# Performance work log

Measured on AMD Instinct MI355X. Metric: run time of the kernel, lower is better.

The kernel has to match this reference:

```python
import jax, jax.numpy as jnp
import numpy as np

IN_CAP_NUM = 1024
IN_CAP_DIM = 64
OUT_CAP_NUM = 32
OUT_CAP_DIM = 64
BATCH = 64
NUM_ITER = 3


def squash(t):
    # t: [..., d]; scale = |t|^2 / (1+|t|^2) / |t|
    sq = jnp.sum(t * t, axis=-1, keepdims=True)
    scale = sq / (1.0 + sq) / jnp.sqrt(sq)
    return scale * t


def setup_inputs() -> dict:
    key = jax.random.key(0)
    k1, k2 = jax.random.split(key)
    x = jax.random.normal(k1, (IN_CAP_NUM, BATCH, IN_CAP_DIM), dtype=jnp.float32)
    route_w = 0.1 * jax.random.normal(
        k2, (OUT_CAP_NUM, IN_CAP_NUM, IN_CAP_DIM, OUT_CAP_DIM), dtype=jnp.float32)
    return {"x": x, "route_w": route_w}


def reference(x, route_w):
    # u[o,i,b,e] = sum_d x[i,b,d] * route_w[o,i,d,e]  (torch broadcast matmul)
    u = jnp.einsum('ibd,oide->oibe', x, route_w)  # [O, I, B, E]
    O = route_w.shape[0]
    b = jnp.zeros((O, 1, 1, 1), dtype=u.dtype)
    v = None
    for it in range(NUM_ITER):
        c = jax.nn.softmax(b, axis=0)                 # coupling over out caps
        s = jnp.sum(c * u, axis=1)                    # [O, B, E]
        v = squash(s)                                 # [O, B, E]
        if it < NUM_ITER - 1:
            # agreement: [O, I, B, 1]
            b = b + jnp.sum(u * v[:, None, :, :], axis=-1, keepdims=True)
    return v
```

## Files before the change

kernel.cpp:

```cpp
#include <hip/hip_runtime.h>
#include <stdint.h>


#define IC 1024
#define OC 32
#define DD 64
#define EE 64
#define BB 64

typedef __attribute__((ext_vector_type(8))) short short8;
typedef __attribute__((ext_vector_type(16))) float f32x16;
typedef _Float16 half8 __attribute__((ext_vector_type(8)));

__device__ __forceinline__ unsigned short f2bf(float f) {
    unsigned int u = __float_as_uint(f);
    u = (u + 0x7FFFu + ((u >> 16) & 1u)) >> 16;
    return (unsigned short)u;
}
__device__ __forceinline__ unsigned int pk2(float a, float b) {
    return (unsigned int)f2bf(a) | ((unsigned int)f2bf(b) << 16);
}

__global__ __launch_bounds__(256)
void u_gemm_kernel(const float* __restrict__ x,
                   const float* __restrict__ w,
                   _Float16* __restrict__ u,
                   float* __restrict__ s_out)
{
    __shared__ unsigned short xs[64 * 68];
    __shared__ unsigned short wT[64 * 68];
    const int t = threadIdx.x;
    const int o = blockIdx.y;
    const int chunk = blockIdx.x;
    const int lane = t & 63;
    const int wv = t >> 6;
    const int bh = wv & 1, eh = wv >> 1;
    const int seg = t & 7;
    const int rrow = t >> 3;

    f32x16 stot = (f32x16)0.0f;

    for (int ii = 0; ii < 32; ++ii) {
        const int i = chunk * 32 + ii;
        __syncthreads();
        for (int hlf = 0; hlf < 2; ++hlf) {
            const int b = rrow + hlf * 32;
            const float* xp = x + (((size_t)i) * BB + b) * DD + seg * 8;
            const float4 xa = *(const float4*)xp;
            const float4 xb = *(const float4*)(xp + 4);
            uint2* dst = (uint2*)&xs[b * 68 + seg * 8];
            dst[0] = make_uint2(pk2(xa.x, xa.y), pk2(xa.z, xa.w));
            dst[1] = make_uint2(pk2(xb.x, xb.y), pk2(xb.z, xb.w));
        }
        {
            const int d0 = rrow * 2;
            const float* wp = w + ((((size_t)o) * IC + i) * DD + d0) * EE + seg * 8;
            const float4 a0 = *(const float4*)(wp);
            const float4 a1 = *(const float4*)(wp + 4);
            const float4 b0 = *(const float4*)(wp + EE);
            const float4 b1 = *(const float4*)(wp + EE + 4);
            const float r0[8] = {a0.x, a0.y, a0.z, a0.w, a1.x, a1.y, a1.z, a1.w};
            const float r1[8] = {b0.x, b0.y, b0.z, b0.w, b1.x, b1.y, b1.z, b1.w};
            #pragma unroll
            for (int j = 0; j < 8; ++j) {
                const int e = seg * 8 + j;
                *(unsigned int*)&wT[e * 68 + d0] = pk2(r0[j], r1[j]);
            }
        }
        __syncthreads();
        f32x16 acc = (f32x16)0.0f;
        #pragma unroll
        for (int kk = 0; kk < 4; ++kk) {
            const int k0 = kk * 16 + (lane >> 5) * 8;
            const int ar = bh * 32 + (lane & 31);
            const int br = eh * 32 + (lane & 31);
            uint2 alo = *(const uint2*)&xs[ar * 68 + k0];
            uint2 ahi = *(const uint2*)&xs[ar * 68 + k0 + 4];
            uint2 blo = *(const uint2*)&wT[br * 68 + k0];
            uint2 bhi = *(const uint2*)&wT[br * 68 + k0 + 4];
            union { uint4 q; short8 s; } au, bu;
            au.q = make_uint4(alo.x, alo.y, ahi.x, ahi.y);
            bu.q = make_uint4(blo.x, blo.y, bhi.x, bhi.y);
            acc = __builtin_amdgcn_mfma_f32_32x32x16_bf16(au.s, bu.s, acc, 0, 0, 0);
        }
        _Float16* ub = u + ((((size_t)o) * IC + i) * BB) * EE;
        #pragma unroll
        for (int r = 0; r < 16; ++r) {
            const int gb = bh * 32 + (r & 3) + 8 * (r >> 2) + 4 * (lane >> 5);
            const int ge = eh * 32 + (lane & 31);
            ub[gb * EE + ge] = (_Float16)acc[r];
            stot[r] += acc[r];
        }
    }
    #pragma unroll
    for (int r = 0; r < 16; ++r) {
        const int gb = bh * 32 + (r & 3) + 8 * (r >> 2) + 4 * (lane >> 5);
        const int ge = eh * 32 + (lane & 31);
        atomicAdd(&s_out[(((size_t)o) * BB + gb) * EE + ge], stot[r] * (1.0f / 32.0f));
    }
}

template<bool FIRST>
__global__ __launch_bounds__(256)
void logits_kernel(const _Float16* __restrict__ u,
                   const float* __restrict__ v,
                   const float* __restrict__ bprev,
                   float* __restrict__ bout,
                   float* __restrict__ cbuf)
{
    __shared__ float Lp[OC][BB];
    const int t = threadIdx.x;
    const int i = blockIdx.x;
    const int b = t >> 2;
    const int eq = t & 3;

    for (int o = 0; o < OC; ++o) {
        const _Float16* up = u + ((((size_t)o) * IC + i) * BB + b) * EE + eq * 16;
        const float*    vp = v + (((size_t)o) * BB + b) * EE + eq * 16;
        const half8 u0 = *(const half8*)up;
        const half8 u1 = *(const half8*)(up + 8);
        const float4 va = *(const float4*)vp;
        const float4 vb = *(const float4*)(vp + 4);
        const float4 vc = *(const float4*)(vp + 8);
        const float4 vd = *(const float4*)(vp + 12);
        float p = (float)u0[0]*va.x + (float)u0[1]*va.y + (float)u0[2]*va.z + (float)u0[3]*va.w
                + (float)u0[4]*vb.x + (float)u0[5]*vb.y + (float)u0[6]*vb.z + (float)u0[7]*vb.w
                + (float)u1[0]*vc.x + (float)u1[1]*vc.y + (float)u1[2]*vc.z + (float)u1[3]*vc.w
                + (float)u1[4]*vd.x + (float)u1[5]*vd.y + (float)u1[6]*vd.z + (float)u1[7]*vd.w;
        p += __shfl_xor(p, 1);
        p += __shfl_xor(p, 2);
        if (eq == 0) Lp[o][b] = p;
    }
    __syncthreads();
    if (t < BB) {
        const int bb = t;
        float lt[OC];
        float m = -1e30f;
        #pragma unroll
        for (int o = 0; o < OC; ++o) {
            float L = Lp[o][bb];
            if (!FIRST) L += bprev[(((size_t)o) * IC + i) * BB + bb];
            if (FIRST)  bout[(((size_t)o) * IC + i) * BB + bb] = L;
            lt[o] = L;
            m = fmaxf(m, L);
        }
        float Z = 0.f;
        #pragma unroll
        for (int o = 0; o < OC; ++o) { lt[o] = __expf(lt[o] - m); Z += lt[o]; }
        const float rZ = 1.0f / Z;
        #pragma unroll
        for (int o = 0; o < OC; ++o)
            cbuf[(((size_t)o) * IC + i) * BB + bb] = lt[o] * rZ;
    }
}

__global__ __launch_bounds__(256)
void sweight_kernel(const _Float16* __restrict__ u,
                    const float* __restrict__ cbuf,
                    float* __restrict__ s_out)
{
    const int t = threadIdx.x;
    const int chunk = blockIdx.x;
    const int o = blockIdx.y;
    const int b = t >> 2;
    const int eq = t & 3;
    float acc[16];
    #pragma unroll
    for (int j = 0; j < 16; ++j) acc[j] = 0.f;
    const int i0 = chunk * 32;
    for (int ii = 0; ii < 32; ++ii) {
        const int i = i0 + ii;
        const float c = cbuf[(((size_t)o) * IC + i) * BB + b];
        const _Float16* up = u + ((((size_t)o) * IC + i) * BB + b) * EE + eq * 16;
        const half8 u0 = *(const half8*)up;
        const half8 u1 = *(const half8*)(up + 8);
        #pragma unroll
        for (int j = 0; j < 8; ++j) acc[j]     += c * (float)u0[j];
        #pragma unroll
        for (int j = 0; j < 8; ++j) acc[8 + j] += c * (float)u1[j];
    }
    float* sp = s_out + (((size_t)o) * BB + b) * EE + eq * 16;
    #pragma unroll
    for (int j = 0; j < 16; ++j) atomicAdd(&sp[j], acc[j]);
}

__global__ __launch_bounds__(256)
void squash_kernel(const float* __restrict__ s, float* __restrict__ vout)
{
    const int o = blockIdx.x;
    const int lane = threadIdx.x & 63;
    const int wv = threadIdx.x >> 6;
    for (int b = wv; b < BB; b += 4) {
        const size_t idx = (((size_t)o) * BB + b) * EE + lane;
        const float val = s[idx];
        float sq = val * val;
        #pragma unroll
        for (int off = 1; off < 64; off <<= 1)
            sq += __shfl_xor(sq, off);
        const float r = sqrtf(sq);
        vout[idx] = val * (r / (1.0f + sq));
    }
}

extern "C" void kernel_launch(void* const* d_in, const int* in_sizes, int n_in,
                              void* d_out, int out_size, void* d_ws, size_t ws_size,
                              hipStream_t stream)
{
    const float* x = (const float*)d_in[0];
    const float* w = (const float*)d_in[1];
    float* out = (float*)d_out;

    char* ws = (char*)d_ws;
    float*    s_buf = (float*)ws;
    float*    vbuf  = (float*)(ws + (1 << 19));
    float*    b1    = (float*)(ws + (1 << 20));
    float*    cbuf  = (float*)(ws + (1 << 20) + (8 << 20));
    _Float16* u     = (_Float16*)(ws + (17u << 20));

    const dim3 blk(256);

    hipMemsetAsync(s_buf, 0, 1 << 19, stream);
    u_gemm_kernel<<<dim3(32, 32), blk, 0, stream>>>(x, w, u, s_buf);
    squash_kernel<<<32, blk, 0, stream>>>(s_buf, vbuf);
    logits_kernel<true><<<1024, blk, 0, stream>>>(u, vbuf, nullptr, b1, cbuf);
    hipMemsetAsync(s_buf, 0, 1 << 19, stream);
    sweight_kernel<<<dim3(32, 32), blk, 0, stream>>>(u, cbuf, s_buf);
    squash_kernel<<<32, blk, 0, stream>>>(s_buf, vbuf);
    logits_kernel<false><<<1024, blk, 0, stream>>>(u, vbuf, b1, nullptr, cbuf);
    hipMemsetAsync(s_buf, 0, 1 << 19, stream);
    sweight_kernel<<<dim3(32, 32), blk, 0, stream>>>(u, cbuf, s_buf);
    squash_kernel<<<32, blk, 0, stream>>>(s_buf, out);
}
```

Before: 1.415 ms.

## Double-buffer GEMM staging, fuse squash into logits, split sweight chunks

The u GEMM kernel now double-buffers its shared-memory tiles and prefetches the next input's x/w registers while the current tile's MFMAs run. The intermediate squash kernels are removed: the logits kernel recomputes the squash scale from s inline and software-pipelines its per-output loads. The weighted-sum kernel uses 16-input chunks with preloaded coefficients and a doubled grid, giving more parallelism at the cost of more atomics. The trade-offs are higher register pressure and redundant norm computation per block.

```diff
diff --git a/kernel.cpp b/kernel.cpp
--- a/kernel.cpp
+++ b/kernel.cpp
@@ -27,8 +27,8 @@
                    _Float16* __restrict__ u,
                    float* __restrict__ s_out)
 {
-    __shared__ unsigned short xs[64 * 68];
-    __shared__ unsigned short wT[64 * 68];
+    __shared__ unsigned short xs[2][64 * 68];
+    __shared__ unsigned short wT[2][64 * 68];
     const int t = threadIdx.x;
     const int o = blockIdx.y;
     const int chunk = blockIdx.x;
@@ -37,60 +37,73 @@
     const int bh = wv & 1, eh = wv >> 1;
     const int seg = t & 7;
     const int rrow = t >> 3;
+    const int d0 = rrow * 2;
+    const int ar = bh * 32 + (lane & 31);
+    const int br = eh * 32 + (lane & 31);
 
     f32x16 stot = (f32x16)0.0f;
 
-    for (int ii = 0; ii < 32; ++ii) {
-        const int i = chunk * 32 + ii;
+#define LOADSET(i_, X0,X1,X2,X3, W0,W1,W2,W3) do {                          \
+    const float* xp = x + (((size_t)(i_)) * BB + rrow) * DD + seg * 8;      \
+    X0 = *(const float4*)xp;            X1 = *(const float4*)(xp + 4);      \
+    X2 = *(const float4*)(xp + 32*DD);  X3 = *(const float4*)(xp + 32*DD+4);\
+    const float* wp = w + ((((size_t)o) * IC + (i_)) * DD + d0) * EE + seg*8;\
+    W0 = *(const float4*)wp;            W1 = *(const float4*)(wp + 4);      \
+    W2 = *(const float4*)(wp + EE);     W3 = *(const float4*)(wp + EE + 4); \
+} while(0)
+
+#define STAGESET(bf_, X0,X1,X2,X3, W0,W1,W2,W3) do {                        \
+    uint2* dx0 = (uint2*)&xs[bf_][rrow * 68 + seg * 8];                     \
+    dx0[0] = make_uint2(pk2(X0.x, X0.y), pk2(X0.z, X0.w));                  \
+    dx0[1] = make_uint2(pk2(X1.x, X1.y), pk2(X1.z, X1.w));                  \
+    uint2* dx1 = (uint2*)&xs[bf_][(rrow + 32) * 68 + seg * 8];              \
+    dx1[0] = make_uint2(pk2(X2.x, X2.y), pk2(X2.z, X2.w));                  \
+    dx1[1] = make_uint2(pk2(X3.x, X3.y), pk2(X3.z, X3.w));                  \
+    const float r0_[8] = {W0.x,W0.y,W0.z,W0.w,W1.x,W1.y,W1.z,W1.w};         \
+    const float r1_[8] = {W2.x,W2.y,W2.z,W2.w,W3.x,W3.y,W3.z,W3.w};         \
+    _Pragma("unroll")                                                       \
+    for (int j = 0; j < 8; ++j)                                             \
+        *(unsigned int*)&wT[bf_][(seg * 8 + j) * 68 + d0] = pk2(r0_[j], r1_[j]); \
+} while(0)
+
+#define MFMA_STORE(bf_, i_) do {                                            \
+    f32x16 acc = (f32x16)0.0f;                                              \
+    _Pragma("unroll")                                                       \
+    for (int kk = 0; kk < 4; ++kk) {                                        \
+        const int k0 = kk * 16 + (lane >> 5) * 8;                           \
+        uint2 alo = *(const uint2*)&xs[bf_][ar * 68 + k0];                  \
+        uint2 ahi = *(const uint2*)&xs[bf_][ar * 68 + k0 + 4];              \
+        uint2 blo = *(const uint2*)&wT[bf_][br * 68 + k0];                  \
+        uint2 bhi = *(const uint2*)&wT[bf_][br * 68 + k0 + 4];              \
+        union { uint4 q; short8 s; } au, bu;                                \
+        au.q = make_uint4(alo.x, alo.y, ahi.x, ahi.y);                      \
+        bu.q = make_uint4(blo.x, blo.y, bhi.x, bhi.y);                      \
+        acc = __builtin_amdgcn_mfma_f32_32x32x16_bf16(au.s, bu.s, acc, 0, 0, 0); \
+    }                                                                       \
+    _Float16* ubp = u + ((((size_t)o) * IC + (i_)) * BB) * EE;              \
+    _Pragma("unroll")                                                       \
+    for (int r = 0; r < 16; ++r) {                                          \
+        const int gb = bh * 32 + (r & 3) + 8 * (r >> 2) + 4 * (lane >> 5);  \
+        const int ge = eh * 32 + (lane & 31);                               \
+        ubp[gb * EE + ge] = (_Float16)acc[r];                               \
+        stot[r] += acc[r];                                                  \
+    }                                                                       \
+} while(0)
+
+    float4 XA0,XA1,XA2,XA3, WA0,WA1,WA2,WA3;
+    float4 XB0,XB1,XB2,XB3, WB0,WB1,WB2,WB3;
+    const int i0 = chunk * 32;
+    LOADSET(i0, XA0,XA1,XA2,XA3, WA0,WA1,WA2,WA3);
+    for (int ii = 0; ii < 32; ii += 2) {
+        STAGESET(0, XA0,XA1,XA2,XA3, WA0,WA1,WA2,WA3);
+        LOADSET(i0 + ii + 1, XB0,XB1,XB2,XB3, WB0,WB1,WB2,WB3);
         __syncthreads();
-        for (int hlf = 0; hlf < 2; ++hlf) {
-            const int b = rrow + hlf * 32;
-            const float* xp = x + (((size_t)i) * BB + b) * DD + seg * 8;
-            const float4 xa = *(const float4*)xp;
-            const float4 xb = *(const float4*)(xp + 4);
-            uint2* dst = (uint2*)&xs[b * 68 + seg * 8];
-            dst[0] = make_uint2(pk2(xa.x, xa.y), pk2(xa.z, xa.w));
-            dst[1] = make_uint2(pk2(xb.x, xb.y), pk2(xb.z, xb.w));
-        }
-        {
-            const int d0 = rrow * 2;
-            const float* wp = w + ((((size_t)o) * IC + i) * DD + d0) * EE + seg * 8;
-            const float4 a0 = *(const float4*)(wp);
-            const float4 a1 = *(const float4*)(wp + 4);
-            const float4 b0 = *(const float4*)(wp + EE);
-            const float4 b1 = *(const float4*)(wp + EE + 4);
-            const float r0[8] = {a0.x, a0.y, a0.z, a0.w, a1.x, a1.y, a1.z, a1.w};
-            const float r1[8] = {b0.x, b0.y, b0.z, b0.w, b1.x, b1.y, b1.z, b1.w};
-            #pragma unroll
-            for (int j = 0; j < 8; ++j) {
-                const int e = seg * 8 + j;
-                *(unsigned int*)&wT[e * 68 + d0] = pk2(r0[j], r1[j]);
-            }
-        }
+        MFMA_STORE(0, i0 + ii);
+        STAGESET(1, XB0,XB1,XB2,XB3, WB0,WB1,WB2,WB3);
+        if (ii + 2 < 32)
+            LOADSET(i0 + ii + 2, XA0,XA1,XA2,XA3, WA0,WA1,WA2,WA3);
         __syncthreads();
-        f32x16 acc = (f32x16)0.0f;
-        #pragma unroll
-        for (int kk = 0; kk < 4; ++kk) {
-            const int k0 = kk * 16 + (lane >> 5) * 8;
-            const int ar = bh * 32 + (lane & 31);
-            const int br = eh * 32 + (lane & 31);
-            uint2 alo = *(const uint2*)&xs[ar * 68 + k0];
-            uint2 ahi = *(const uint2*)&xs[ar * 68 + k0 + 4];
-            uint2 blo = *(const uint2*)&wT[br * 68 + k0];
-            uint2 bhi = *(const uint2*)&wT[br * 68 + k0 + 4];
-            union { uint4 q; short8 s; } au, bu;
-            au.q = make_uint4(alo.x, alo.y, ahi.x, ahi.y);
-            bu.q = make_uint4(blo.x, blo.y, bhi.x, bhi.y);
-            acc = __builtin_amdgcn_mfma_f32_32x32x16_bf16(au.s, bu.s, acc, 0, 0, 0);
-        }
-        _Float16* ub = u + ((((size_t)o) * IC + i) * BB) * EE;
-        #pragma unroll
-        for (int r = 0; r < 16; ++r) {
-            const int gb = bh * 32 + (r & 3) + 8 * (r >> 2) + 4 * (lane >> 5);
-            const int ge = eh * 32 + (lane & 31);
-            ub[gb * EE + ge] = (_Float16)acc[r];
-            stot[r] += acc[r];
-        }
+        MFMA_STORE(1, i0 + ii + 1);
     }
     #pragma unroll
     for (int r = 0; r < 16; ++r) {
@@ -98,12 +111,15 @@
         const int ge = eh * 32 + (lane & 31);
         atomicAdd(&s_out[(((size_t)o) * BB + gb) * EE + ge], stot[r] * (1.0f / 32.0f));
     }
+#undef LOADSET
+#undef STAGESET
+#undef MFMA_STORE
 }
 
 template<bool FIRST>
 __global__ __launch_bounds__(256)
 void logits_kernel(const _Float16* __restrict__ u,
-                   const float* __restrict__ v,
+                   const float* __restrict__ s,
                    const float* __restrict__ bprev,
                    float* __restrict__ bout,
                    float* __restrict__ cbuf)
@@ -113,23 +129,52 @@
     const int i = blockIdx.x;
     const int b = t >> 2;
     const int eq = t & 3;
-
-    for (int o = 0; o < OC; ++o) {
-        const _Float16* up = u + ((((size_t)o) * IC + i) * BB + b) * EE + eq * 16;
-        const float*    vp = v + (((size_t)o) * BB + b) * EE + eq * 16;
-        const half8 u0 = *(const half8*)up;
-        const half8 u1 = *(const half8*)(up + 8);
-        const float4 va = *(const float4*)vp;
-        const float4 vb = *(const float4*)(vp + 4);
-        const float4 vc = *(const float4*)(vp + 8);
-        const float4 vd = *(const float4*)(vp + 12);
-        float p = (float)u0[0]*va.x + (float)u0[1]*va.y + (float)u0[2]*va.z + (float)u0[3]*va.w
-                + (float)u0[4]*vb.x + (float)u0[5]*vb.y + (float)u0[6]*vb.z + (float)u0[7]*vb.w
-                + (float)u1[0]*vc.x + (float)u1[1]*vc.y + (float)u1[2]*vc.z + (float)u1[3]*vc.w
-                + (float)u1[4]*vd.x + (float)u1[5]*vd.y + (float)u1[6]*vd.z + (float)u1[7]*vd.w;
+    const size_t OSU = (size_t)IC * BB * EE;
+    const _Float16* up = u + (((size_t)i) * BB + b) * EE + eq * 16;
+    const float*    sp = s + ((size_t)b) * EE + eq * 16;
+
+    half8 uA0, uA1, uB0, uB1;
+    float4 sA0, sA1, sA2, sA3, sB0, sB1, sB2, sB3;
+
+    auto ldA = [&](int o) {
+        const _Float16* p = up + (size_t)o * OSU;
+        uA0 = *(const half8*)p; uA1 = *(const half8*)(p + 8);
+        const float* q = sp + (size_t)o * (BB * EE);
+        sA0 = *(const float4*)q;      sA1 = *(const float4*)(q + 4);
+        sA2 = *(const float4*)(q + 8); sA3 = *(const float4*)(q + 12);
+    };
+    auto ldB = [&](int o) {
+        const _Float16* p = up + (size_t)o * OSU;
+        uB0 = *(const half8*)p; uB1 = *(const half8*)(p + 8);
+        const float* q = sp + (size_t)o * (BB * EE);
+        sB0 = *(const float4*)q;      sB1 = *(const float4*)(q + 4);
+        sB2 = *(const float4*)(q + 8); sB3 = *(const float4*)(q + 12);
+    };
+    auto body = [&](half8 u0, half8 u1, float4 v0, float4 v1, float4 v2,
+                    float4 v3, int o) {
+        float sq = v0.x*v0.x + v0.y*v0.y + v0.z*v0.z + v0.w*v0.w
+                 + v1.x*v1.x + v1.y*v1.y + v1.z*v1.z + v1.w*v1.w
+                 + v2.x*v2.x + v2.y*v2.y + v2.z*v2.z + v2.w*v2.w
+                 + v3.x*v3.x + v3.y*v3.y + v3.z*v3.z + v3.w*v3.w;
+        sq += __shfl_xor(sq, 1);
+        sq += __shfl_xor(sq, 2);
+        const float scale = sqrtf(sq) / (1.0f + sq);
+        float p = (float)u0[0]*v0.x + (float)u0[1]*v0.y + (float)u0[2]*v0.z + (float)u0[3]*v0.w
+                + (float)u0[4]*v1.x + (float)u0[5]*v1.y + (float)u0[6]*v1.z + (float)u0[7]*v1.w
+                + (float)u1[0]*v2.x + (float)u1[1]*v2.y + (float)u1[2]*v2.z + (float)u1[3]*v2.w
+                + (float)u1[4]*v3.x + (float)u1[5]*v3.y + (float)u1[6]*v3.z + (float)u1[7]*v3.w;
+        p *= scale;
         p += __shfl_xor(p, 1);
         p += __shfl_xor(p, 2);
         if (eq == 0) Lp[o][b] = p;
+    };
+
+    ldA(0);
+    for (int o = 0; o < OC; o += 2) {
+        ldB(o + 1);
+        body(uA0, uA1, sA0, sA1, sA2, sA3, o);
+        if (o + 2 < OC) ldA(o + 2);
+        body(uB0, uB1, sB0, sB1, sB2, sB3, o + 1);
     }
     __syncthreads();
     if (t < BB) {
@@ -164,20 +209,26 @@
     const int o = blockIdx.y;
     const int b = t >> 2;
     const int eq = t & 3;
+    const int i0 = chunk * 16;
+
+    float c[16];
+    #pragma unroll
+    for (int j = 0; j < 16; ++j)
+        c[j] = cbuf[(((size_t)o) * IC + i0 + j) * BB + b];
+
     float acc[16];
     #pragma unroll
     for (int j = 0; j < 16; ++j) acc[j] = 0.f;
-    const int i0 = chunk * 32;
-    for (int ii = 0; ii < 32; ++ii) {
-        const int i = i0 + ii;
-        const float c = cbuf[(((size_t)o) * IC + i) * BB + b];
-        const _Float16* up = u + ((((size_t)o) * IC + i) * BB + b) * EE + eq * 16;
-        const half8 u0 = *(const half8*)up;
-        const half8 u1 = *(const half8*)(up + 8);
-        #pragma unroll
-        for (int j = 0; j < 8; ++j) acc[j]     += c * (float)u0[j];
-        #pragma unroll
-        for (int j = 0; j < 8; ++j) acc[8 + j] += c * (float)u1[j];
+
+    const _Float16* up = u + ((((size_t)o) * IC + i0) * BB + b) * EE + eq * 16;
+    #pragma unroll
+    for (int ii = 0; ii < 16; ++ii) {
+        const half8 u0 = *(const half8*)(up + (size_t)ii * (BB * EE));
+        const half8 u1 = *(const half8*)(up + (size_t)ii * (BB * EE) + 8);
+        #pragma unroll
+        for (int j = 0; j < 8; ++j) acc[j]     += c[ii] * (float)u0[j];
+        #pragma unroll
+        for (int j = 0; j < 8; ++j) acc[8 + j] += c[ii] * (float)u1[j];
     }
     float* sp = s_out + (((size_t)o) * BB + b) * EE + eq * 16;
     #pragma unroll
@@ -212,7 +263,6 @@
 
     char* ws = (char*)d_ws;
     float*    s_buf = (float*)ws;
-    float*    vbuf  = (float*)(ws + (1 << 19));
     float*    b1    = (float*)(ws + (1 << 20));
     float*    cbuf  = (float*)(ws + (1 << 20) + (8 << 20));
     _Float16* u     = (_Float16*)(ws + (17u << 20));
@@ -221,13 +271,11 @@
 
     hipMemsetAsync(s_buf, 0, 1 << 19, stream);
     u_gemm_kernel<<<dim3(32, 32), blk, 0, stream>>>(x, w, u, s_buf);
-    squash_kernel<<<32, blk, 0, stream>>>(s_buf, vbuf);
-    logits_kernel<true><<<1024, blk, 0, stream>>>(u, vbuf, nullptr, b1, cbuf);
+    logits_kernel<true><<<1024, blk, 0, stream>>>(u, s_buf, nullptr, b1, cbuf);
     hipMemsetAsync(s_buf, 0, 1 << 19, stream);
-    sweight_kernel<<<dim3(32, 32), blk, 0, stream>>>(u, cbuf, s_buf);
-    squash_kernel<<<32, blk, 0, stream>>>(s_buf, vbuf);
-    logits_kernel<false><<<1024, blk, 0, stream>>>(u, vbuf, b1, nullptr, cbuf);
+    sweight_kernel<<<dim3(64, 32), blk, 0, stream>>>(u, cbuf, s_buf);
+    logits_kernel<false><<<1024, blk, 0, stream>>>(u, s_buf, b1, nullptr, cbuf);
     hipMemsetAsync(s_buf, 0, 1 << 19, stream);
-    sweight_kernel<<<dim3(32, 32), blk, 0, stream>>>(u, cbuf, s_buf);
+    sweight_kernel<<<dim3(64, 32), blk, 0, stream>>>(u, cbuf, s_buf);
     squash_kernel<<<32, blk, 0, stream>>>(s_buf, out);
 }
```

After: 1.822 ms. +28.7%, slower.
